# Optimization experiments

Measured on AMD Instinct MI355X. Metric: run time of the kernel, lower is better.

Reference implementation:

```python
import jax, jax.numpy as jnp
import numpy as np

N, E, G = 15000, 150000, 64
FN, FE, FS, OUT = 64, 16, 128, 2
H1, C1 = 4, 128
H2, C2 = 4, 256
EPS = 1e-5


def _bn(x, g, b):
    # BatchNorm1d forward with batch statistics
    m = jnp.mean(x, 0)
    v = jnp.var(x, 0)
    return g * (x - m) / jnp.sqrt(v + EPS) + b


def _tconv(x, src, dst, edge_attr, Wq, bq, Wk, bk, Wv, bv, We, Wskip, bskip, heads, ch, n):
    # PyG TransformerConv: gather -> edge attention -> segment softmax -> scatter
    q = (x @ Wq + bq).reshape(-1, heads, ch)            # [N,H,C]
    k = (x @ Wk + bk).reshape(-1, heads, ch)
    v = (x @ Wv + bv).reshape(-1, heads, ch)
    e = (edge_attr @ We).reshape(-1, heads, ch)          # [E,H,C]
    k_e = k[src] + e                                     # [E,H,C]
    alpha = jnp.sum(q[dst] * k_e, axis=-1) / jnp.sqrt(jnp.float32(ch))  # [E,H]
    amax = jax.ops.segment_max(alpha, dst, num_segments=n)              # [N,H]
    ex = jnp.exp(alpha - amax[dst])
    den = jax.ops.segment_sum(ex, dst, num_segments=n)
    a = ex / (den[dst] + 1e-16)                          # [E,H]
    msg = (v[src] + e) * a[..., None]                    # [E,H,C]
    out = jax.ops.segment_sum(msg, dst, num_segments=n).reshape(-1, heads * ch)
    return out + x @ Wskip + bskip                       # root/skip connection


def setup_inputs() -> dict:
    ks = jax.random.split(jax.random.key(0), 32)
    s = 0.05
    d = {}
    d['x'] = jax.random.normal(ks[0], (N, FN), jnp.float32)
    d['edge_attr'] = jax.random.normal(ks[1], (E, FE), jnp.float32)
    d['solvent_fingerprint'] = jax.random.uniform(ks[2], (G, FS), jnp.float32)
    d['edge_index'] = jax.random.randint(ks[3], (2, E), 0, N)
    d['batch'] = jnp.sort(jax.random.randint(ks[4], (N,), 0, G))
    HC1, HC2 = H1 * C1, H2 * C2
    d['Wq1'] = jax.random.normal(ks[5], (FN, HC1)) * s; d['bq1'] = jnp.zeros((HC1,))
    d['Wk1'] = jax.random.normal(ks[6], (FN, HC1)) * s; d['bk1'] = jnp.zeros((HC1,))
    d['Wv1'] = jax.random.normal(ks[7], (FN, HC1)) * s; d['bv1'] = jnp.zeros((HC1,))
    d['We1'] = jax.random.normal(ks[8], (FE, HC1)) * s
    d['Wskip1'] = jax.random.normal(ks[9], (FN, HC1)) * s; d['bskip1'] = jnp.zeros((HC1,))
    d['bn1_g'] = jnp.ones((HC1,)); d['bn1_b'] = jnp.zeros((HC1,))
    d['Wq2'] = jax.random.normal(ks[10], (HC1, HC2)) * s; d['bq2'] = jnp.zeros((HC2,))
    d['Wk2'] = jax.random.normal(ks[11], (HC1, HC2)) * s; d['bk2'] = jnp.zeros((HC2,))
    d['Wv2'] = jax.random.normal(ks[12], (HC1, HC2)) * s; d['bv2'] = jnp.zeros((HC2,))
    d['We2'] = jax.random.normal(ks[13], (FE, HC2)) * s
    d['Wskip2'] = jax.random.normal(ks[14], (HC1, HC2)) * s; d['bskip2'] = jnp.zeros((HC2,))
    d['bn2_g'] = jnp.ones((HC2,)); d['bn2_b'] = jnp.zeros((HC2,))
    d['Wsol'] = jax.random.normal(ks[15], (FS, 128)) * s; d['bsol'] = jnp.zeros((128,))
    d['Wfc1'] = jax.random.normal(ks[16], (HC2 * 2 + 128, 128)) * s; d['bfc1'] = jnp.zeros((128,))
    d['bnf_g'] = jnp.ones((128,)); d['bnf_b'] = jnp.zeros((128,))
    d['Wfc2'] = jax.random.normal(ks[17], (128, OUT)) * s; d['bfc2'] = jnp.zeros((OUT,))
    return d


def reference(x, edge_attr, solvent_fingerprint, edge_index, batch,
              Wq1, bq1, Wk1, bk1, Wv1, bv1, We1, Wskip1, bskip1, bn1_g, bn1_b,
              Wq2, bq2, Wk2, bk2, Wv2, bv2, We2, Wskip2, bskip2, bn2_g, bn2_b,
              Wsol, bsol, Wfc1, bfc1, bnf_g, bnf_b, Wfc2, bfc2):
    src, dst = edge_index[0], edge_index[1]
    h = _tconv(x, src, dst, edge_attr, Wq1, bq1, Wk1, bk1, Wv1, bv1, We1, Wskip1, bskip1, H1, C1, N)
    h = jax.nn.relu(_bn(h, bn1_g, bn1_b))
    h = _tconv(h, src, dst, edge_attr, Wq2, bq2, Wk2, bk2, Wv2, bv2, We2, Wskip2, bskip2, H2, C2, N)
    h = jax.nn.relu(_bn(h, bn2_g, bn2_b))
    # global mean / max pooling over graphs
    cnt = jax.ops.segment_sum(jnp.ones((N,), h.dtype), batch, num_segments=G)
    gap = jax.ops.segment_sum(h, batch, num_segments=G) / jnp.maximum(cnt, 1.0)[:, None]
    gmp = jax.ops.segment_max(h, batch, num_segments=G)
    gmp = jnp.where(jnp.isfinite(gmp), gmp, 0.0)
    sol = jax.nn.relu(solvent_fingerprint @ Wsol + bsol)
    z = jnp.concatenate([gap, gmp, sol], axis=1)
    z = jax.nn.relu(_bn(z @ Wfc1 + bfc1, bnf_g, bnf_b))  # dropout = identity (eval)
    return z @ Wfc2 + bfc2
```

## Files before the change

### kernel.cpp

```cpp
#include <hip/hip_runtime.h>
#include <cstdint>
#include <cstddef>

#define DEV __device__ __forceinline__

static constexpr int NN = 15000;
static constexpr int EE = 150000;
static constexpr int GG = 64;

typedef __attribute__((ext_vector_type(8))) short bf16x8;
typedef __attribute__((ext_vector_type(4))) float f32x4;

DEV short f2b1(float f) {
    unsigned u = __float_as_uint(f);
    unsigned r = (u + 0x7fffu + ((u >> 16) & 1u)) >> 16;
    return (short)r;
}
DEV float b2f(short s) { return __uint_as_float(((unsigned)(unsigned short)s) << 16); }

template <bool BIAS, bool ACCUM, bool BF16OUT>
__global__ __launch_bounds__(256) void gemm_mfma(const short* __restrict__ A,
                                                 const short* __restrict__ Bt,
                                                 const float* __restrict__ bias,
                                                 void* __restrict__ Cv, int M, int N,
                                                 int K) {
    __shared__ short As[128 * 32];
    __shared__ short Bs[128 * 32];
    const int tid = threadIdx.x;
    const int wid = tid >> 6, lane = tid & 63;
    const int wr = wid >> 1, wc = wid & 1;
    const int row0 = blockIdx.y * 128, col0 = blockIdx.x * 128;

    const int o0 = wid * 2, o1 = wid * 2 + 1;
    const int rA0 = o0 * 16 + (lane >> 2), rA1 = o1 * 16 + (lane >> 2);
    const int c0 = (lane & 3) ^ ((rA0 >> 1) & 3);
    const int c1 = (lane & 3) ^ ((rA1 >> 1) & 3);
    const short* gA0 = A + (size_t)(row0 + rA0) * K + c0 * 8;
    const short* gA1 = A + (size_t)(row0 + rA1) * K + c1 * 8;
    const short* gB0 = Bt + (size_t)(col0 + rA0) * K + c0 * 8;
    const short* gB1 = Bt + (size_t)(col0 + rA1) * K + c1 * 8;
    const bool okA0 = (row0 + rA0) < M, okA1 = (row0 + rA1) < M;

    f32x4 acc[4][4] = {};
    for (int k0 = 0; k0 < K; k0 += 32) {
        if (okA0) __builtin_amdgcn_global_load_lds(gA0 + k0, &As[o0 * 512], 16, 0, 0);
        if (okA1) __builtin_amdgcn_global_load_lds(gA1 + k0, &As[o1 * 512], 16, 0, 0);
        __builtin_amdgcn_global_load_lds(gB0 + k0, &Bs[o0 * 512], 16, 0, 0);
        __builtin_amdgcn_global_load_lds(gB1 + k0, &Bs[o1 * 512], 16, 0, 0);
        __syncthreads();
        const int kg4 = lane >> 4;
        bf16x8 af[4], bfv[4];
#pragma unroll
        for (int m = 0; m < 4; m++) {
            int ar = wr * 64 + m * 16 + (lane & 15);
            af[m] = *(const bf16x8*)&As[ar * 32 + (kg4 ^ ((ar >> 1) & 3)) * 8];
        }
#pragma unroll
        for (int n = 0; n < 4; n++) {
            int br = wc * 64 + n * 16 + (lane & 15);
            bfv[n] = *(const bf16x8*)&Bs[br * 32 + (kg4 ^ ((br >> 1) & 3)) * 8];
        }
#pragma unroll
        for (int m = 0; m < 4; m++)
#pragma unroll
            for (int n = 0; n < 4; n++)
                acc[m][n] = __builtin_amdgcn_mfma_f32_16x16x32_bf16(af[m], bfv[n],
                                                                   acc[m][n], 0, 0, 0);
        __syncthreads();
    }
    const int colb = col0 + wc * 64 + (lane & 15);
    const int rowb = row0 + wr * 64 + (lane >> 4) * 4;
    float* Cf = (float*)Cv;
    short* Cb = (short*)Cv;
#pragma unroll
    for (int n = 0; n < 4; n++) {
        int gc = colb + n * 16;
        float bv = BIAS ? bias[gc] : 0.f;
#pragma unroll
        for (int m = 0; m < 4; m++) {
            int gr = rowb + m * 16;
#pragma unroll
            for (int r = 0; r < 4; r++) {
                if (gr + r < M) {
                    float v = acc[m][n][r] + bv;
                    if constexpr (ACCUM) v += Cf[(size_t)(gr + r) * N + gc];
                    if constexpr (BF16OUT)
                        Cb[(size_t)(gr + r) * N + gc] = f2b1(v);
                    else
                        Cf[(size_t)(gr + r) * N + gc] = v;
                }
            }
        }
    }
}

__global__ __launch_bounds__(256) void gemm_mfma_n64(const short* __restrict__ A,
                                                     const short* __restrict__ Bt,
                                                     const float* __restrict__ bias,
                                                     float* __restrict__ C, int M,
                                                     int K) {
    __shared__ short As[256][40];
    __shared__ short Bs[64][40];
    const int tid = threadIdx.x;
    const int wid = tid >> 6, lane = tid & 63;
    const int row0 = blockIdx.x * 256;
    f32x4 acc[4][4] = {};
    for (int k0 = 0; k0 < K; k0 += 32) {
        {
            int gr = row0 + tid;
            bf16x8 v0 = {}, v1 = {}, v2 = {}, v3 = {};
            if (gr < M) {
                const short* src = A + (size_t)gr * K + k0;
                v0 = *(const bf16x8*)(src);
                v1 = *(const bf16x8*)(src + 8);
                v2 = *(const bf16x8*)(src + 16);
                v3 = *(const bf16x8*)(src + 24);
            }
            *(bf16x8*)&As[tid][0] = v0;
            *(bf16x8*)&As[tid][8] = v1;
            *(bf16x8*)&As[tid][16] = v2;
            *(bf16x8*)&As[tid][24] = v3;
        }
        {
            int r = tid >> 2, c8 = (tid & 3) * 8;
            *(bf16x8*)&Bs[r][c8] = *(const bf16x8*)(Bt + (size_t)r * K + k0 + c8);
        }
        __syncthreads();
        const int kg = (lane >> 4) * 8;
        bf16x8 af[4], bfr[4];
#pragma unroll
        for (int m = 0; m < 4; m++)
            af[m] = *(const bf16x8*)&As[wid * 64 + m * 16 + (lane & 15)][kg];
#pragma unroll
        for (int n = 0; n < 4; n++)
            bfr[n] = *(const bf16x8*)&Bs[n * 16 + (lane & 15)][kg];
#pragma unroll
        for (int m = 0; m < 4; m++)
#pragma unroll
            for (int n = 0; n < 4; n++)
                acc[m][n] = __builtin_amdgcn_mfma_f32_16x16x32_bf16(af[m], bfr[n],
                                                                   acc[m][n], 0, 0, 0);
        __syncthreads();
    }
    const int colb = lane & 15;
    const int rowb = row0 + wid * 64 + (lane >> 4) * 4;
#pragma unroll
    for (int n = 0; n < 4; n++) {
        int gc = colb + n * 16;
        float bv = bias[gc];
#pragma unroll
        for (int m = 0; m < 4; m++) {
            int gr = rowb + m * 16;
#pragma unroll
            for (int r = 0; r < 4; r++)
                if (gr + r < M) C[(size_t)(gr + r) * 64 + gc] = acc[m][n][r] + bv;
        }
    }
}

template <int C, int K>
__global__ __launch_bounds__(256) void wqu_combine(const float* __restrict__ Wq,
                                                   const float* __restrict__ We,
                                                   short* __restrict__ out) {
    int i = blockIdx.x * 256 + threadIdx.x;
    if (i >= 64 * K) return;
    int hf = i / K, kk = i - hf * K;
    int h = hf >> 4, f = hf & 15;
    const float* wq = Wq + (size_t)kk * (4 * C) + h * C;
    const float* we = We + (size_t)f * (4 * C) + h * C;
    float s0 = 0.f, s1 = 0.f, s2 = 0.f, s3 = 0.f;
    for (int c = 0; c < C; c += 4) {
        float4 a = *(const float4*)(wq + c);
        float4 b = *(const float4*)(we + c);
        s0 = fmaf(a.x, b.x, s0);
        s1 = fmaf(a.y, b.y, s1);
        s2 = fmaf(a.z, b.z, s2);
        s3 = fmaf(a.w, b.w, s3);
    }
    out[i] = f2b1((s0 + s1) + (s2 + s3));
}
template <int C>
__global__ void bu_combine(const float* __restrict__ bq, const float* __restrict__ We,
                           float* __restrict__ bu) {
    int hf = threadIdx.x;
    int h = hf >> 4, f = hf & 15;
    float s = 0.f;
    for (int c = 0; c < C; c++) s = fmaf(bq[h * C + c], We[(size_t)f * 4 * C + h * C + c], s);
    bu[hf] = s;
}

template <bool RELU>
__global__ __launch_bounds__(256) void gemm_row(const float* __restrict__ A,
                                                const float* __restrict__ B,
                                                const float* __restrict__ bias,
                                                float* __restrict__ C, int N, int K,
                                                int lda, int ldc) {
    int g = blockIdx.x;
    int col = threadIdx.x & 127;
    int half = threadIdx.x >> 7;
    int kh = K >> 1;
    int k0 = half * kh, k1 = k0 + kh;
    const float* a = A + (size_t)g * lda;
    float s0 = 0.f, s1 = 0.f, s2 = 0.f, s3 = 0.f;
    int kk = k0;
    for (; kk + 4 <= k1; kk += 4) {
        s0 = fmaf(a[kk], B[(size_t)kk * N + col], s0);
        s1 = fmaf(a[kk + 1], B[(size_t)(kk + 1) * N + col], s1);
        s2 = fmaf(a[kk + 2], B[(size_t)(kk + 2) * N + col], s2);
        s3 = fmaf(a[kk + 3], B[(size_t)(kk + 3) * N + col], s3);
    }
    for (; kk < k1; kk++) s0 = fmaf(a[kk], B[(size_t)kk * N + col], s0);
    float s = (s0 + s1) + (s2 + s3);
    __shared__ float red[128];
    if (half == 1) red[col] = s;
    __syncthreads();
    if (half == 0) {
        s += red[col] + bias[col];
        if (RELU) s = fmaxf(s, 0.f);
        C[(size_t)g * ldc + col] = s;
    }
}

__global__ __launch_bounds__(256) void gemm_row_part(const float* __restrict__ A,
                                                     const float* __restrict__ B,
                                                     float* __restrict__ P, int K,
                                                     int lda, int chunk) {
    int g = blockIdx.x, s = blockIdx.y;
    int col = threadIdx.x & 127, half = threadIdx.x >> 7;
    int kb = s * chunk + half * (chunk >> 1);
    int ke = min(kb + (chunk >> 1), K);
    const float* a = A + (size_t)g * lda;
    float s0 = 0.f, s1 = 0.f, s2 = 0.f, s3 = 0.f;
    int kk = kb;
    for (; kk + 4 <= ke; kk += 4) {
        s0 = fmaf(a[kk], B[(size_t)kk * 128 + col], s0);
        s1 = fmaf(a[kk + 1], B[(size_t)(kk + 1) * 128 + col], s1);
        s2 = fmaf(a[kk + 2], B[(size_t)(kk + 2) * 128 + col], s2);
        s3 = fmaf(a[kk + 3], B[(size_t)(kk + 3) * 128 + col], s3);
    }
    for (; kk < ke; kk++) s0 = fmaf(a[kk], B[(size_t)kk * 128 + col], s0);
    float v = (s0 + s1) + (s2 + s3);
    __shared__ float red[128];
    if (half == 1) red[col] = v;
    __syncthreads();
    if (half == 0) P[((size_t)s * 64 + g) * 128 + col] = v + red[col];
}
__global__ __launch_bounds__(128) void gemm_row_reduce(const float* __restrict__ P,
                                                       const float* __restrict__ bias,
                                                       float* __restrict__ C, int nsplit) {
    int g = blockIdx.x, col = threadIdx.x;
    float sum = bias[col];
    for (int s = 0; s < nsplit; s++) sum += P[((size_t)s * 64 + g) * 128 + col];
    C[(size_t)g * 128 + col] = sum;
}

__global__ __launch_bounds__(256) void f2b_vec(const float* __restrict__ in,
                                               short* __restrict__ out, int n4) {
    int i = blockIdx.x * 256 + threadIdx.x;
    if (i >= n4) return;
    float4 v = ((const float4*)in)[i];
    short4 o;
    o.x = f2b1(v.x); o.y = f2b1(v.y); o.z = f2b1(v.z); o.w = f2b1(v.w);
    ((short4*)out)[i] = o;
}
__global__ __launch_bounds__(256) void f2b_T(const float* __restrict__ in,
                                             short* __restrict__ out, int K, int N) {
    __shared__ short tile[32][33];
    int kb = blockIdx.y * 32, nb = blockIdx.x * 32;
    int tx = threadIdx.x & 31, ty = threadIdx.x >> 5;
#pragma unroll
    for (int i = 0; i < 32; i += 8) {
        int kk = kb + ty + i, n = nb + tx;
        if (kk < K && n < N) tile[ty + i][tx] = f2b1(in[(size_t)kk * N + n]);
    }
    __syncthreads();
#pragma unroll
    for (int i = 0; i < 32; i += 8) {
        int n = nb + ty + i, kk = kb + tx;
        if (n < N && kk < K) out[(size_t)n * K + kk] = tile[tx][ty + i];
    }
}
template <int D, int C>
__global__ __launch_bounds__(256) void build_wub(const float* __restrict__ We,
                                                 short* __restrict__ out) {
    int i = blockIdx.x * 256 + threadIdx.x;
    if (i >= D * 64) return;
    int d = i >> 6, hf = i & 63;
    int hp = hf >> 4, f = hf & 15;
    float v = ((d / C) == hp) ? We[(size_t)f * D + d] : 0.f;
    out[i] = f2b1(v);
}

__global__ __launch_bounds__(256) void count_deg(const int* __restrict__ dst,
                                                 int* __restrict__ deg, int E) {
    int e = blockIdx.x * 256 + threadIdx.x;
    if (e < E) atomicAdd(&deg[dst[e]], 1);
}

__global__ __launch_bounds__(1024) void scan_deg(const int* __restrict__ deg,
                                                 int* __restrict__ rs,
                                                 int* __restrict__ cursor, int n) {
    __shared__ int part[1024];
    int t = threadIdx.x;
    int ch = (n + 1023) / 1024;
    int b0 = min(t * ch, n), b1 = min(b0 + ch, n);
    int s = 0;
    for (int i = b0; i < b1; i++) s += deg[i];
    part[t] = s;
    __syncthreads();
    for (int off = 1; off < 1024; off <<= 1) {
        int tmp = (t >= off) ? part[t - off] : 0;
        __syncthreads();
        part[t] += tmp;
        __syncthreads();
    }
    int run = part[t] - s;
    for (int i = b0; i < b1; i++) {
        rs[i] = run;
        cursor[i] = run;
        run += deg[i];
    }
    if (t == 1023) rs[n] = part[1023];
}

__global__ __launch_bounds__(256) void fill_csr(const int* __restrict__ dst,
                                                int* __restrict__ cursor,
                                                int* __restrict__ eids, int E) {
    int e = blockIdx.x * 256 + threadIdx.x;
    if (e < E) {
        int pos = atomicAdd(&cursor[dst[e]], 1);
        eids[pos] = e;
    }
}

template <int C>
__global__ __launch_bounds__(256) void node_alpha(
    const short* __restrict__ q, const short* __restrict__ k,
    const float* __restrict__ U, const float* __restrict__ ea,
    const int* __restrict__ src, const int* __restrict__ rs,
    const int* __restrict__ eids, float* __restrict__ ab,
    float* __restrict__ den, int Nn) {
    constexpr int D = 4 * C;
    constexpr int P = D / 64;
    int node = (blockIdx.x * 256 + threadIdx.x) >> 6;
    int lane = threadIdx.x & 63;
    if (node >= Nn) return;
    int e0 = rs[node], e1 = rs[node + 1];
    float qr[P];
    const short* qp = q + (size_t)node * D + lane * P;
#pragma unroll
    for (int j0 = 0; j0 < P; j0 += 8) {
        bf16x8 v = *(const bf16x8*)(qp + j0);
#pragma unroll
        for (int j = 0; j < 8; j++) qr[j0 + j] = b2f(v[j]);
    }
    float Urow = U[(size_t)node * 64 + lane];
    const float rsC = rsqrtf((float)C);
    float m = -3.402823466e38f;
    for (int ii = e0; ii < e1; ii++) {
        int e = eids[ii];
        int s = src[e];
        float val = ea[(size_t)e * 16 + (lane & 15)] * Urow;
        const short* kp = k + (size_t)s * D + lane * P;
#pragma unroll
        for (int j0 = 0; j0 < P; j0 += 8) {
            bf16x8 kv = *(const bf16x8*)(kp + j0);
#pragma unroll
            for (int j = 0; j < 8; j++) val = fmaf(qr[j0 + j], b2f(kv[j]), val);
        }
#pragma unroll
        for (int off = 1; off < 16; off <<= 1) val += __shfl_xor(val, off);
        val *= rsC;
        if ((lane & 15) == 0) ab[(size_t)ii * 4 + (lane >> 4)] = val;
        m = fmaxf(m, val);
    }
    float dsum = 0.f;
    for (int ii = e0; ii < e1; ii++) {
        float a = ab[(size_t)ii * 4 + (lane >> 4)];
        float ex = __expf(a - m);
        dsum += ex;
        if ((lane & 15) == 0) ab[(size_t)ii * 4 + (lane >> 4)] = ex;
    }
    if ((lane & 15) == 0) den[(size_t)node * 4 + (lane >> 4)] = dsum;
}

template <int C>
__global__ __launch_bounds__(256) void node_scatter(
    const short* __restrict__ v, const float* __restrict__ ea,
    const int* __restrict__ src, const int* __restrict__ rs,
    const int* __restrict__ eids, const float* __restrict__ ab,
    const float* __restrict__ den, float* __restrict__ hout,
    short* __restrict__ Tb, int Nn) {
    constexpr int D = 4 * C;
    constexpr int P = D / 64;
    int node = (blockIdx.x * 256 + threadIdx.x) >> 6;
    int lane = threadIdx.x & 63;
    if (node >= Nn) return;
    int e0 = rs[node], e1 = rs[node + 1];
    float acc[P] = {};
    float tacc = 0.f;
    for (int ii = e0; ii < e1; ii++) {
        int e = eids[ii];
        int s = src[e];
        float ex = ab[(size_t)ii * 4 + (lane >> 4)];
        tacc = fmaf(ex, ea[(size_t)e * 16 + (lane & 15)], tacc);
        const short* vp = v + (size_t)s * D + lane * P;
#pragma unroll
        for (int j0 = 0; j0 < P; j0 += 8) {
            bf16x8 t8 = *(const bf16x8*)(vp + j0);
#pragma unroll
            for (int j = 0; j < 8; j++) acc[j0 + j] = fmaf(ex, b2f(t8[j]), acc[j0 + j]);
        }
    }
    float inv = 1.f / (den[(size_t)node * 4 + (lane >> 4)] + 1e-16f);
    Tb[(size_t)node * 64 + lane] = f2b1(tacc * inv);
    float* hp = hout + (size_t)node * D + lane * P;
#pragma unroll
    for (int j = 0; j < P; j += 4) {
        float4 t4 = *(float4*)(hp + j);
        t4.x = fmaf(acc[j], inv, t4.x);
        t4.y = fmaf(acc[j + 1], inv, t4.y);
        t4.z = fmaf(acc[j + 2], inv, t4.z);
        t4.w = fmaf(acc[j + 3], inv, t4.w);
        *(float4*)(hp + j) = t4;
    }
}

__global__ __launch_bounds__(256) void bn_stats(const float* __restrict__ h,
                                                float* __restrict__ s1,
                                                float* __restrict__ s2, int Nrows,
                                                int D) {
    int col = blockIdx.x * 256 + threadIdx.x;
    int chunk = (Nrows + gridDim.y - 1) / gridDim.y;
    int r0 = blockIdx.y * chunk;
    int r1 = min(r0 + chunk, Nrows);
    float a = 0.f, b = 0.f;
    for (int r = r0; r < r1; r++) {
        float v = h[(size_t)r * D + col];
        a += v;
        b += v * v;
    }
    atomicAdd(&s1[col], a);
    atomicAdd(&s2[col], b);
}
__global__ void bn_finalize(float* __restrict__ s1, float* __restrict__ s2,
                            const float* __restrict__ g, const float* __restrict__ b,
                            int Nrows, int D) {
    int c = blockIdx.x * 256 + threadIdx.x;
    if (c >= D) return;
    float mean = s1[c] / (float)Nrows;
    float var = fmaxf(s2[c] / (float)Nrows - mean * mean, 0.f);
    float scale = g[c] / sqrtf(var + 1e-5f);
    s1[c] = scale;
    s2[c] = b[c] - mean * scale;
}
__global__ __launch_bounds__(256) void bn_apply_relu_f32(float* __restrict__ h,
                                                         const float* __restrict__ scale,
                                                         const float* __restrict__ shift,
                                                         int total4, int D) {
    int i = blockIdx.x * 256 + threadIdx.x;
    if (i >= total4) return;
    float4 v = ((float4*)h)[i];
    int c = (i * 4) % D;
    v.x = fmaxf(fmaf(v.x, scale[c], shift[c]), 0.f);
    v.y = fmaxf(fmaf(v.y, scale[c + 1], shift[c + 1]), 0.f);
    v.z = fmaxf(fmaf(v.z, scale[c + 2], shift[c + 2]), 0.f);
    v.w = fmaxf(fmaf(v.w, scale[c + 3], shift[c + 3]), 0.f);
    ((float4*)h)[i] = v;
}
__global__ __launch_bounds__(256) void bn_apply_relu_b16(const float* __restrict__ h,
                                                         const float* __restrict__ scale,
                                                         const float* __restrict__ shift,
                                                         short* __restrict__ out,
                                                         int total4, int D) {
    int i = blockIdx.x * 256 + threadIdx.x;
    if (i >= total4) return;
    float4 v = ((const float4*)h)[i];
    int c = (i * 4) % D;
    short4 o;
    o.x = f2b1(fmaxf(fmaf(v.x, scale[c], shift[c]), 0.f));
    o.y = f2b1(fmaxf(fmaf(v.y, scale[c + 1], shift[c + 1]), 0.f));
    o.z = f2b1(fmaxf(fmaf(v.z, scale[c + 2], shift[c + 2]), 0.f));
    o.w = f2b1(fmaxf(fmaf(v.w, scale[c + 3], shift[c + 3]), 0.f));
    ((short4*)out)[i] = o;
}

__global__ __launch_bounds__(256) void pool_kernel(const float* __restrict__ h,
                                                   const int* __restrict__ batch,
                                                   float* __restrict__ z, int Nrows,
                                                   int D, int ldz) {
    int g = blockIdx.y;
    int c = blockIdx.x * 256 + threadIdx.x;
    int lo = 0, hi = Nrows;
    while (lo < hi) {
        int m = (lo + hi) >> 1;
        if (batch[m] < g) lo = m + 1; else hi = m;
    }
    int s0 = lo;
    hi = Nrows;
    while (lo < hi) {
        int m = (lo + hi) >> 1;
        if (batch[m] < g + 1) lo = m + 1; else hi = m;
    }
    int s1 = lo;
    float sum = 0.f, mx = -3.402823466e38f;
    for (int r = s0; r < s1; r++) {
        float v = h[(size_t)r * D + c];
        sum += v;
        mx = fmaxf(mx, v);
    }
    int cnt = s1 - s0;
    z[(size_t)g * ldz + c] = sum / (float)max(cnt, 1);
    z[(size_t)g * ldz + D + c] = (cnt > 0) ? mx : 0.f;
}

__global__ __launch_bounds__(128) void bn_small_apply(const float* __restrict__ y,
                                                      const float* __restrict__ g,
                                                      const float* __restrict__ b,
                                                      float* __restrict__ y2) {
    int c = threadIdx.x;
    float m = 0.f;
    for (int r = 0; r < 64; r++) m += y[r * 128 + c];
    m *= (1.f / 64.f);
    float v = 0.f;
    for (int r = 0; r < 64; r++) {
        float d = y[r * 128 + c] - m;
        v += d * d;
    }
    v *= (1.f / 64.f);
    float sc = g[c] / sqrtf(v + 1e-5f);
    float sh = b[c] - m * sc;
    for (int r = 0; r < 64; r++) y2[r * 128 + c] = fmaxf(fmaf(y[r * 128 + c], sc, sh), 0.f);
}
__global__ __launch_bounds__(128) void fc2_small(const float* __restrict__ y2,
                                                 const float* __restrict__ W,
                                                 const float* __restrict__ b,
                                                 float* __restrict__ out) {
    int t = threadIdx.x;
    int g = t >> 1, o = t & 1;
    float s = b[o];
    for (int kk = 0; kk < 128; kk++) s = fmaf(y2[g * 128 + kk], W[kk * 2 + o], s);
    out[g * 2 + o] = s;
}

extern "C" void kernel_launch(void* const* d_in, const int* in_sizes, int n_in,
                              void* d_out, int out_size, void* d_ws, size_t ws_size,
                              hipStream_t stream) {
    const float* x     = (const float*)d_in[0];
    const float* ea    = (const float*)d_in[1];
    const float* sol   = (const float*)d_in[2];
    const int*   eidx  = (const int*)d_in[3];
    const int*   batch = (const int*)d_in[4];
    const float* Wq1 = (const float*)d_in[5];  const float* bq1 = (const float*)d_in[6];
    const float* Wk1 = (const float*)d_in[7];  const float* bk1 = (const float*)d_in[8];
    const float* Wv1 = (const float*)d_in[9];  const float* bv1 = (const float*)d_in[10];
    const float* We1 = (const float*)d_in[11];
    const float* Ws1 = (const float*)d_in[12]; const float* bs1 = (const float*)d_in[13];
    const float* g1  = (const float*)d_in[14]; const float* be1 = (const float*)d_in[15];
    const float* Wq2 = (const float*)d_in[16]; const float* bq2 = (const float*)d_in[17];
    const float* Wk2 = (const float*)d_in[18]; const float* bk2 = (const float*)d_in[19];
    const float* Wv2 = (const float*)d_in[20]; const float* bv2 = (const float*)d_in[21];
    const float* We2 = (const float*)d_in[22];
    const float* Ws2 = (const float*)d_in[23]; const float* bs2 = (const float*)d_in[24];
    const float* g2  = (const float*)d_in[25]; const float* be2 = (const float*)d_in[26];
    const float* Wsol = (const float*)d_in[27]; const float* bsol = (const float*)d_in[28];
    const float* Wfc1 = (const float*)d_in[29]; const float* bfc1 = (const float*)d_in[30];
    const float* gf   = (const float*)d_in[31]; const float* bf = (const float*)d_in[32];
    const float* Wfc2 = (const float*)d_in[33]; const float* bfc2 = (const float*)d_in[34];

    const int* srcp = eidx;
    const int* dstp = eidx + EE;

    char* p = (char*)d_ws;
    auto alloc = [&](size_t bytes) -> char* {
        char* r = p;
        p += (bytes + 255) & ~(size_t)255;
        return r;
    };
    float* R0   = (float*)alloc((size_t)NN * 1024 * 4);
    short* h1b  = (short*)alloc((size_t)NN * 512 * 2);
    short* bufAb = (short*)alloc((size_t)NN * 1024 * 2);
    short* bufBb = (short*)alloc((size_t)NN * 1024 * 2);
    float* U    = (float*)alloc((size_t)NN * 64 * 4);
    short* Tb   = (short*)alloc((size_t)NN * 64 * 2);
    float* ab   = (float*)alloc((size_t)EE * 4 * 4);
    float* den  = (float*)alloc((size_t)NN * 4 * 4);
    short* wub  = (short*)alloc((size_t)1024 * 64 * 2);
    short* wq1t = (short*)alloc((size_t)512 * 64 * 2);
    short* wk1t = (short*)alloc((size_t)512 * 64 * 2);
    short* wv1t = (short*)alloc((size_t)512 * 64 * 2);
    short* ws1t = (short*)alloc((size_t)512 * 64 * 2);
    short* wq2t = (short*)alloc((size_t)1024 * 512 * 2);
    short* wk2t = (short*)alloc((size_t)1024 * 512 * 2);
    short* wv2t = (short*)alloc((size_t)1024 * 512 * 2);
    short* ws2t = (short*)alloc((size_t)1024 * 512 * 2);
    short* xb   = (short*)alloc((size_t)NN * 64 * 2);
    short* wqu1t = (short*)alloc((size_t)64 * 64 * 2);
    short* wqu2t = (short*)alloc((size_t)64 * 512 * 2);
    float* bu1  = (float*)alloc(64 * 4);
    float* bu2  = (float*)alloc(64 * 4);
    int* deg    = (int*)alloc((size_t)NN * 4);
    int* cursor = (int*)alloc((size_t)NN * 4);
    int* rs     = (int*)alloc((size_t)(NN + 1) * 4);
    int* eids   = (int*)alloc((size_t)EE * 4);
    float* bnA  = (float*)alloc(1024 * 4);
    float* bnB  = (float*)alloc(1024 * 4);
    float* z  = (float*)alloc((size_t)64 * 2176 * 4);
    float* y  = (float*)alloc((size_t)64 * 128 * 4);
    float* y2 = (float*)alloc((size_t)64 * 128 * 4);
    float* yP = (float*)alloc((size_t)17 * 64 * 128 * 4);
    if ((size_t)(p - (char*)d_ws) > ws_size) return;

    float* h1 = R0;
    float* h2 = R0;

    const int GRM = (NN + 127) / 128;
    const int GRU = (NN + 255) / 256;
    const int NWB = (NN * 64 + 255) / 256;
    dim3 blk(256);

    hipMemsetAsync(deg, 0, (size_t)NN * 4, stream);
    count_deg<<<(EE + 255) / 256, blk, 0, stream>>>(dstp, deg, EE);
    scan_deg<<<1, 1024, 0, stream>>>(deg, rs, cursor, NN);
    fill_csr<<<(EE + 255) / 256, blk, 0, stream>>>(dstp, cursor, eids, EE);

    f2b_vec<<<(NN * 64 / 4 + 255) / 256, blk, 0, stream>>>(x, xb, NN * 64 / 4);
    f2b_T<<<dim3(512 / 32, 2), blk, 0, stream>>>(Wq1, wq1t, 64, 512);
    f2b_T<<<dim3(512 / 32, 2), blk, 0, stream>>>(Wk1, wk1t, 64, 512);
    f2b_T<<<dim3(512 / 32, 2), blk, 0, stream>>>(Wv1, wv1t, 64, 512);
    f2b_T<<<dim3(512 / 32, 2), blk, 0, stream>>>(Ws1, ws1t, 64, 512);
    f2b_T<<<dim3(1024 / 32, 512 / 32), blk, 0, stream>>>(Wq2, wq2t, 512, 1024);
    f2b_T<<<dim3(1024 / 32, 512 / 32), blk, 0, stream>>>(Wk2, wk2t, 512, 1024);
    f2b_T<<<dim3(1024 / 32, 512 / 32), blk, 0, stream>>>(Wv2, wv2t, 512, 1024);
    f2b_T<<<dim3(1024 / 32, 512 / 32), blk, 0, stream>>>(Ws2, ws2t, 512, 1024);
    wqu_combine<128, 64><<<(64 * 64 + 255) / 256, blk, 0, stream>>>(Wq1, We1, wqu1t);
    wqu_combine<256, 512><<<(64 * 512 + 255) / 256, blk, 0, stream>>>(Wq2, We2, wqu2t);
    bu_combine<128><<<1, 64, 0, stream>>>(bq1, We1, bu1);
    bu_combine<256><<<1, 64, 0, stream>>>(bq2, We2, bu2);

    hipMemsetAsync(bnA, 0, 1024 * 4, stream);
    hipMemsetAsync(bnB, 0, 1024 * 4, stream);

    gemm_mfma<true, false, true><<<dim3(4, GRM), blk, 0, stream>>>(xb, wq1t, bq1, bufAb, NN, 512, 64);
    gemm_mfma<true, false, true><<<dim3(4, GRM), blk, 0, stream>>>(xb, wk1t, bk1, bufBb, NN, 512, 64);
    gemm_mfma_n64<<<GRU, blk, 0, stream>>>(xb, wqu1t, bu1, U, NN, 64);
    node_alpha<128><<<NWB, blk, 0, stream>>>(bufAb, bufBb, U, ea, srcp, rs, eids, ab, den, NN);
    gemm_mfma<true, false, true><<<dim3(4, GRM), blk, 0, stream>>>(xb, wv1t, bv1, bufAb, NN, 512, 64);
    gemm_mfma<true, false, false><<<dim3(4, GRM), blk, 0, stream>>>(xb, ws1t, bs1, h1, NN, 512, 64);
    node_scatter<128><<<NWB, blk, 0, stream>>>(bufAb, ea, srcp, rs, eids, ab, den, h1, Tb, NN);
    build_wub<512, 128><<<(512 * 64 + 255) / 256, blk, 0, stream>>>(We1, wub);
    gemm_mfma<false, true, false><<<dim3(4, GRM), blk, 0, stream>>>(Tb, wub, nullptr, h1, NN, 512, 64);
    bn_stats<<<dim3(2, 64), blk, 0, stream>>>(h1, bnA, bnB, NN, 512);
    bn_finalize<<<2, blk, 0, stream>>>(bnA, bnB, g1, be1, NN, 512);
    bn_apply_relu_b16<<<NN * 512 / 4 / 256, blk, 0, stream>>>(h1, bnA, bnB, h1b, NN * 512 / 4, 512);

    hipMemsetAsync(bnA, 0, 1024 * 4, stream);
    hipMemsetAsync(bnB, 0, 1024 * 4, stream);
    gemm_mfma<true, false, true><<<dim3(8, GRM), blk, 0, stream>>>(h1b, wq2t, bq2, bufAb, NN, 1024, 512);
    gemm_mfma<true, false, true><<<dim3(8, GRM), blk, 0, stream>>>(h1b, wk2t, bk2, bufBb, NN, 1024, 512);
    gemm_mfma_n64<<<GRU, blk, 0, stream>>>(h1b, wqu2t, bu2, U, NN, 512);
    node_alpha<256><<<NWB, blk, 0, stream>>>(bufAb, bufBb, U, ea, srcp, rs, eids, ab, den, NN);
    gemm_mfma<true, false, true><<<dim3(8, GRM), blk, 0, stream>>>(h1b, wv2t, bv2, bufAb, NN, 1024, 512);
    gemm_mfma<true, false, false><<<dim3(8, GRM), blk, 0, stream>>>(h1b, ws2t, bs2, h2, NN, 1024, 512);
    node_scatter<256><<<NWB, blk, 0, stream>>>(bufAb, ea, srcp, rs, eids, ab, den, h2, Tb, NN);
    build_wub<1024, 256><<<(1024 * 64 + 255) / 256, blk, 0, stream>>>(We2, wub);
    gemm_mfma<false, true, false><<<dim3(8, GRM), blk, 0, stream>>>(Tb, wub, nullptr, h2, NN, 1024, 64);
    bn_stats<<<dim3(4, 64), blk, 0, stream>>>(h2, bnA, bnB, NN, 1024);
    bn_finalize<<<4, blk, 0, stream>>>(bnA, bnB, g2, be2, NN, 1024);
    bn_apply_relu_f32<<<NN * 1024 / 4 / 256, blk, 0, stream>>>(h2, bnA, bnB, NN * 1024 / 4, 1024);

    pool_kernel<<<dim3(4, 64), blk, 0, stream>>>(h2, batch, z, NN, 1024, 2176);
    gemm_row<true><<<64, blk, 0, stream>>>(sol, Wsol, bsol, z + 2048, 128, 128, 128, 2176);
    gemm_row_part<<<dim3(64, 17), blk, 0, stream>>>(z, Wfc1, yP, 2176, 2176, 128);
    gemm_row_reduce<<<64, 128, 0, stream>>>(yP, bfc1, y, 17);
    bn_small_apply<<<1, 128, 0, stream>>>(y, gf, bf, y2);
    fc2_small<<<1, 128, 0, stream>>>(y2, Wfc2, bfc2, (float*)d_out);
}
```

Measured before the change: 1.043 ms.

## Fuse Q and K projection GEMMs, parallelize pooling and BN stats

```diff
diff --git a/kernel.cpp b/kernel.cpp
--- a/kernel.cpp
+++ b/kernel.cpp
@@ -23,7 +23,7 @@
                                                  const short* __restrict__ Bt,
                                                  const float* __restrict__ bias,
                                                  void* __restrict__ Cv, int M, int N,
-                                                 int K) {
+                                                 int K, int ldc) {
     __shared__ short As[128 * 32];
     __shared__ short Bs[128 * 32];
     const int tid = threadIdx.x;
@@ -83,11 +83,11 @@
             for (int r = 0; r < 4; r++) {
                 if (gr + r < M) {
                     float v = acc[m][n][r] + bv;
-                    if constexpr (ACCUM) v += Cf[(size_t)(gr + r) * N + gc];
+                    if constexpr (ACCUM) v += Cf[(size_t)(gr + r) * ldc + gc];
                     if constexpr (BF16OUT)
-                        Cb[(size_t)(gr + r) * N + gc] = f2b1(v);
+                        Cb[(size_t)(gr + r) * ldc + gc] = f2b1(v);
                     else
-                        Cf[(size_t)(gr + r) * N + gc] = v;
+                        Cf[(size_t)(gr + r) * ldc + gc] = v;
                 }
             }
         }
@@ -189,6 +189,13 @@
     bu[hf] = s;
 }
 
+__global__ void concat2(const float* __restrict__ a, const float* __restrict__ b,
+                        float* __restrict__ o, int n) {
+    int i = blockIdx.x * 256 + threadIdx.x;
+    if (i < n) o[i] = a[i];
+    else if (i < 2 * n) o[i] = b[i - n];
+}
+
 template <bool RELU>
 __global__ __launch_bounds__(256) void gemm_row(const float* __restrict__ A,
                                                 const float* __restrict__ B,
@@ -335,7 +342,7 @@
 
 template <int C>
 __global__ __launch_bounds__(256) void node_alpha(
-    const short* __restrict__ q, const short* __restrict__ k,
+    const short* __restrict__ q, const short* __restrict__ k, int ld,
     const float* __restrict__ U, const float* __restrict__ ea,
     const int* __restrict__ src, const int* __restrict__ rs,
     const int* __restrict__ eids, float* __restrict__ ab,
@@ -347,7 +354,7 @@
     if (node >= Nn) return;
     int e0 = rs[node], e1 = rs[node + 1];
     float qr[P];
-    const short* qp = q + (size_t)node * D + lane * P;
+    const short* qp = q + (size_t)node * ld + lane * P;
 #pragma unroll
     for (int j0 = 0; j0 < P; j0 += 8) {
         bf16x8 v = *(const bf16x8*)(qp + j0);
@@ -361,7 +368,7 @@
         int e = eids[ii];
         int s = src[e];
         float val = ea[(size_t)e * 16 + (lane & 15)] * Urow;
-        const short* kp = k + (size_t)s * D + lane * P;
+        const short* kp = k + (size_t)s * ld + lane * P;
 #pragma unroll
         for (int j0 = 0; j0 < P; j0 += 8) {
             bf16x8 kv = *(const bf16x8*)(kp + j0);
@@ -386,7 +393,7 @@
 
 template <int C>
 __global__ __launch_bounds__(256) void node_scatter(
-    const short* __restrict__ v, const float* __restrict__ ea,
+    const short* __restrict__ v, int ld, const float* __restrict__ ea,
     const int* __restrict__ src, const int* __restrict__ rs,
     const int* __restrict__ eids, const float* __restrict__ ab,
     const float* __restrict__ den, float* __restrict__ hout,
@@ -404,7 +411,7 @@
         int s = src[e];
         float ex = ab[(size_t)ii * 4 + (lane >> 4)];
         tacc = fmaf(ex, ea[(size_t)e * 16 + (lane & 15)], tacc);
-        const short* vp = v + (size_t)s * D + lane * P;
+        const short* vp = v + (size_t)s * ld + lane * P;
 #pragma unroll
         for (int j0 = 0; j0 < P; j0 += 8) {
             bf16x8 t8 = *(const bf16x8*)(vp + j0);
@@ -490,7 +497,9 @@
                                                    float* __restrict__ z, int Nrows,
                                                    int D, int ldz) {
     int g = blockIdx.y;
-    int c = blockIdx.x * 256 + threadIdx.x;
+    int cl = threadIdx.x & 63;
+    int c = blockIdx.x * 64 + cl;
+    int chunk = threadIdx.x >> 6;
     int lo = 0, hi = Nrows;
     while (lo < hi) {
         int m = (lo + hi) >> 1;
@@ -503,15 +512,29 @@
         if (batch[m] < g + 1) lo = m + 1; else hi = m;
     }
     int s1 = lo;
+    int cnt = s1 - s0;
+    int per = (cnt + 3) >> 2;
+    int r0 = s0 + chunk * per;
+    int r1 = min(r0 + per, s1);
     float sum = 0.f, mx = -3.402823466e38f;
-    for (int r = s0; r < s1; r++) {
+    for (int r = r0; r < r1; r++) {
         float v = h[(size_t)r * D + c];
         sum += v;
         mx = fmaxf(mx, v);
     }
-    int cnt = s1 - s0;
-    z[(size_t)g * ldz + c] = sum / (float)max(cnt, 1);
-    z[(size_t)g * ldz + D + c] = (cnt > 0) ? mx : 0.f;
+    __shared__ float ss[4][64], sm[4][64];
+    ss[chunk][cl] = sum;
+    sm[chunk][cl] = mx;
+    __syncthreads();
+    if (chunk == 0) {
+#pragma unroll
+        for (int j = 1; j < 4; j++) {
+            sum += ss[j][cl];
+            mx = fmaxf(mx, sm[j][cl]);
+        }
+        z[(size_t)g * ldz + c] = sum / (float)max(cnt, 1);
+        z[(size_t)g * ldz + D + c] = (cnt > 0) ? mx : 0.f;
+    }
 }
 
 __global__ __launch_bounds__(128) void bn_small_apply(const float* __restrict__ y,
@@ -581,6 +604,7 @@
     short* h1b  = (short*)alloc((size_t)NN * 512 * 2);
     short* bufAb = (short*)alloc((size_t)NN * 1024 * 2);
     short* bufBb = (short*)alloc((size_t)NN * 1024 * 2);
+    (void)bufBb;
     float* U    = (float*)alloc((size_t)NN * 64 * 4);
     short* Tb   = (short*)alloc((size_t)NN * 64 * 2);
     float* ab   = (float*)alloc((size_t)EE * 4 * 4);
@@ -599,6 +623,8 @@
     short* wqu2t = (short*)alloc((size_t)64 * 512 * 2);
     float* bu1  = (float*)alloc(64 * 4);
     float* bu2  = (float*)alloc(64 * 4);
+    float* bqk1 = (float*)alloc(1024 * 4);
+    float* bqk2 = (float*)alloc(2048 * 4);
     int* deg    = (int*)alloc((size_t)NN * 4);
     int* cursor = (int*)alloc((size_t)NN * 4);
     int* rs     = (int*)alloc((size_t)(NN + 1) * 4);
@@ -637,39 +663,39 @@
     wqu_combine<256, 512><<<(64 * 512 + 255) / 256, blk, 0, stream>>>(Wq2, We2, wqu2t);
     bu_combine<128><<<1, 64, 0, stream>>>(bq1, We1, bu1);
     bu_combine<256><<<1, 64, 0, stream>>>(bq2, We2, bu2);
+    concat2<<<(1024 + 255) / 256, blk, 0, stream>>>(bq1, bk1, bqk1, 512);
+    concat2<<<(2048 + 255) / 256, blk, 0, stream>>>(bq2, bk2, bqk2, 1024);
 
     hipMemsetAsync(bnA, 0, 1024 * 4, stream);
     hipMemsetAsync(bnB, 0, 1024 * 4, stream);
 
-    gemm_mfma<true, false, true><<<dim3(4, GRM), blk, 0, stream>>>(xb, wq1t, bq1, bufAb, NN, 512, 64);
-    gemm_mfma<true, false, true><<<dim3(4, GRM), blk, 0, stream>>>(xb, wk1t, bk1, bufBb, NN, 512, 64);
+    gemm_mfma<true, false, true><<<dim3(8, GRM), blk, 0, stream>>>(xb, wq1t, bqk1, bufAb, NN, 1024, 64, 1024);
     gemm_mfma_n64<<<GRU, blk, 0, stream>>>(xb, wqu1t, bu1, U, NN, 64);
-    node_alpha<128><<<NWB, blk, 0, stream>>>(bufAb, bufBb, U, ea, srcp, rs, eids, ab, den, NN);
-    gemm_mfma<true, false, true><<<dim3(4, GRM), blk, 0, stream>>>(xb, wv1t, bv1, bufAb, NN, 512, 64);
-    gemm_mfma<true, false, false><<<dim3(4, GRM), blk, 0, stream>>>(xb, ws1t, bs1, h1, NN, 512, 64);
-    node_scatter<128><<<NWB, blk, 0, stream>>>(bufAb, ea, srcp, rs, eids, ab, den, h1, Tb, NN);
+    node_alpha<128><<<NWB, blk, 0, stream>>>(bufAb, bufAb + 512, 1024, U, ea, srcp, rs, eids, ab, den, NN);
+    gemm_mfma<true, false, true><<<dim3(4, GRM), blk, 0, stream>>>(xb, wv1t, bv1, bufAb, NN, 512, 64, 1024);
+    gemm_mfma<true, false, false><<<dim3(4, GRM), blk, 0, stream>>>(xb, ws1t, bs1, h1, NN, 512, 64, 512);
+    node_scatter<128><<<NWB, blk, 0, stream>>>(bufAb, 1024, ea, srcp, rs, eids, ab, den, h1, Tb, NN);
     build_wub<512, 128><<<(512 * 64 + 255) / 256, blk, 0, stream>>>(We1, wub);
-    gemm_mfma<false, true, false><<<dim3(4, GRM), blk, 0, stream>>>(Tb, wub, nullptr, h1, NN, 512, 64);
-    bn_stats<<<dim3(2, 64), blk, 0, stream>>>(h1, bnA, bnB, NN, 512);
+    gemm_mfma<false, true, false><<<dim3(4, GRM), blk, 0, stream>>>(Tb, wub, nullptr, h1, NN, 512, 64, 512);
+    bn_stats<<<dim3(2, 256), blk, 0, stream>>>(h1, bnA, bnB, NN, 512);
     bn_finalize<<<2, blk, 0, stream>>>(bnA, bnB, g1, be1, NN, 512);
     bn_apply_relu_b16<<<NN * 512 / 4 / 256, blk, 0, stream>>>(h1, bnA, bnB, h1b, NN * 512 / 4, 512);
 
     hipMemsetAsync(bnA, 0, 1024 * 4, stream);
     hipMemsetAsync(bnB, 0, 1024 * 4, stream);
-    gemm_mfma<true, false, true><<<dim3(8, GRM), blk, 0, stream>>>(h1b, wq2t, bq2, bufAb, NN, 1024, 512);
-    gemm_mfma<true, false, true><<<dim3(8, GRM), blk, 0, stream>>>(h1b, wk2t, bk2, bufBb, NN, 1024, 512);
+    gemm_mfma<true, false, true><<<dim3(16, GRM), blk, 0, stream>>>(h1b, wq2t, bqk2, bufAb, NN, 2048, 512, 2048);
     gemm_mfma_n64<<<GRU, blk, 0, stream>>>(h1b, wqu2t, bu2, U, NN, 512);
-    node_alpha<256><<<NWB, blk, 0, stream>>>(bufAb, bufBb, U, ea, srcp, rs, eids, ab, den, NN);
-    gemm_mfma<true, false, true><<<dim3(8, GRM), blk, 0, stream>>>(h1b, wv2t, bv2, bufAb, NN, 1024, 512);
-    gemm_mfma<true, false, false><<<dim3(8, GRM), blk, 0, stream>>>(h1b, ws2t, bs2, h2, NN, 1024, 512);
-    node_scatter<256><<<NWB, blk, 0, stream>>>(bufAb, ea, srcp, rs, eids, ab, den, h2, Tb, NN);
+    node_alpha<256><<<NWB, blk, 0, stream>>>(bufAb, bufAb + 1024, 2048, U, ea, srcp, rs, eids, ab, den, NN);
+    gemm_mfma<true, false, true><<<dim3(8, GRM), blk, 0, stream>>>(h1b, wv2t, bv2, bufAb, NN, 1024, 512, 2048);
+    gemm_mfma<true, false, false><<<dim3(8, GRM), blk, 0, stream>>>(h1b, ws2t, bs2, h2, NN, 1024, 512, 1024);
+    node_scatter<256><<<NWB, blk, 0, stream>>>(bufAb, 2048, ea, srcp, rs, eids, ab, den, h2, Tb, NN);
     build_wub<1024, 256><<<(1024 * 64 + 255) / 256, blk, 0, stream>>>(We2, wub);
-    gemm_mfma<false, true, false><<<dim3(8, GRM), blk, 0, stream>>>(Tb, wub, nullptr, h2, NN, 1024, 64);
-    bn_stats<<<dim3(4, 64), blk, 0, stream>>>(h2, bnA, bnB, NN, 1024);
+    gemm_mfma<false, true, false><<<dim3(8, GRM), blk, 0, stream>>>(Tb, wub, nullptr, h2, NN, 1024, 64, 1024);
+    bn_stats<<<dim3(4, 256), blk, 0, stream>>>(h2, bnA, bnB, NN, 1024);
     bn_finalize<<<4, blk, 0, stream>>>(bnA, bnB, g2, be2, NN, 1024);
     bn_apply_relu_f32<<<NN * 1024 / 4 / 256, blk, 0, stream>>>(h2, bnA, bnB, NN * 1024 / 4, 1024);
 
-    pool_kernel<<<dim3(4, 64), blk, 0, stream>>>(h2, batch, z, NN, 1024, 2176);
+    pool_kernel<<<dim3(16, 64), blk, 0, stream>>>(h2, batch, z, NN, 1024, 2176);
     gemm_row<true><<<64, blk, 0, stream>>>(sol, Wsol, bsol, z + 2048, 128, 128, 128, 2176);
     gemm_row_part<<<dim3(64, 17), blk, 0, stream>>>(z, Wfc1, yP, 2176, 2176, 128);
     gemm_row_reduce<<<64, 128, 0, stream>>>(yP, bfc1, y, 17);
```

Result: faster. 900.1 us (-13.7%).
